# Performance work log

Measured on AMD Instinct MI355X. Metric: run time of the kernel, lower is better.

## Reference

```python
import jax, jax.numpy as jnp
import numpy as np

D_MODEL = 1024
NHEAD = 16
HEAD_DIM = D_MODEL // NHEAD
SCALE = 1.0 / np.sqrt(HEAD_DIM).astype(np.float32)
B, L = 2, 2048
NEG_INF = -1e30


def setup_inputs() -> dict:
    key = jax.random.key(0)
    ks = jax.random.split(key, 12)
    xav = np.sqrt(6.0 / (D_MODEL + D_MODEL)).astype(np.float32)  # xavier_uniform gain=1
    def lin_w(k):
        return jax.random.uniform(k, (D_MODEL, D_MODEL), jnp.float32, -xav, xav)
    x = jax.random.normal(ks[0], (B, L, D_MODEL), jnp.float32)
    role_mask = jax.random.randint(ks[1], (B, L), 0, 2, jnp.int32)
    # causal attention mask: True = masked (upper triangle above diagonal)
    attn_mask = jnp.triu(jnp.ones((L, L), jnp.bool_), k=1)
    # random key padding: True = padded key
    key_padding_mask = jax.random.randint(ks[2], (B, L), 0, 2, jnp.int32).astype(jnp.bool_)
    return {
        "x": x,
        "role_mask": role_mask,
        "attn_mask": attn_mask,
        "key_padding_mask": key_padding_mask,
        "Wq": lin_w(ks[3]), "bq": jnp.zeros((D_MODEL,), jnp.float32),
        "Wk": lin_w(ks[4]), "bk": jnp.zeros((D_MODEL,), jnp.float32),
        "Wv": lin_w(ks[5]), "bv": jnp.zeros((D_MODEL,), jnp.float32),
        "Wo": lin_w(ks[6]), "bo": jnp.zeros((D_MODEL,), jnp.float32),
        "delta": jnp.asarray(1.0, jnp.float32),
    }


def reference(x, role_mask, attn_mask, key_padding_mask,
              Wq, bq, Wk, bk, Wv, bv, Wo, bo, delta):
    Bb, Ll, Dd = x.shape
    def heads(t):  # [B,L,D] -> [B,H,L,hd]
        return t.reshape(Bb, Ll, NHEAD, HEAD_DIM).transpose(0, 2, 1, 3)
    Q = heads(x @ Wq.T + bq)
    K = heads(x @ Wk.T + bk)
    V = heads(x @ Wv.T + bv)
    scores = jnp.einsum('bhqd,bhkd->bhqk', Q, K) * SCALE  # [B,H,L,L]
    same_role = (role_mask[:, :, None] == role_mask[:, None, :])  # [B,L,L]
    scores = scores + (same_role.astype(scores.dtype) * delta)[:, None, :, :]
    scores = jnp.where(attn_mask[None, None, :, :], -jnp.inf, scores)
    scores = jnp.where(key_padding_mask[:, None, None, :], -jnp.inf, scores)
    attn = jax.nn.softmax(scores, axis=-1)
    attn = jnp.nan_to_num(attn, nan=0.0, posinf=0.0, neginf=0.0)
    out = jnp.einsum('bhqk,bhkd->bhqd', attn, V)
    out = out.transpose(0, 2, 1, 3).reshape(Bb, Ll, Dd)
    return out @ Wo.T + bo
```

## Files before the change

kernel.cpp:

```cpp
#include <hip/hip_runtime.h>
#include <hip/hip_bf16.h>

#define DM 1024
#define NH 16
#define HD 64
#define BB 2
#define LL 2048
#define SCALE 0.125f
#define NEG_BIG -1e30f
#define LOG2E 1.4426950408889634f
#define SC2 (SCALE * LOG2E)
#define FIXM 16.0f
#define SLOTB 8448
#define POOL0_SLOTS 960

typedef __bf16 bf16;
typedef __bf16 bf16x8 __attribute__((ext_vector_type(8)));
typedef __bf16 bf16x4 __attribute__((ext_vector_type(4)));
typedef float f32x4 __attribute__((ext_vector_type(4)));

static __device__ inline bf16x8 load8(const bf16* p) {
    return *reinterpret_cast<const bf16x8*>(p);
}

static __device__ inline float scrub(float x) {
    union { float f; unsigned u; } c; c.f = x;
    return ((c.u & 0x7F800000u) == 0x7F800000u) ? 0.f : x;
}

typedef __attribute__((address_space(1))) const unsigned char ga_t;
typedef __attribute__((address_space(3))) unsigned char ls_t;
static __device__ inline void gload_lds16(const void* g, void* l) {
    __builtin_amdgcn_global_load_lds((ga_t*)g, (ls_t*)l, 16, 0, 0);
}

__global__ __launch_bounds__(256) void prep_all(
    const float* __restrict__ x,
    const float* __restrict__ Wq, const float* __restrict__ Wk,
    const float* __restrict__ Wv, const float* __restrict__ Wo,
    bf16* __restrict__ xb, bf16* __restrict__ Wqb, bf16* __restrict__ Wkb,
    bf16* __restrict__ Wvb, bf16* __restrict__ Wob,
    const int* __restrict__ role, const void* __restrict__ kpad,
    const float* __restrict__ deltap, float2* __restrict__ biasG)
{
    const int tid = threadIdx.x;
    const int gid = blockIdx.x;
    if (gid < 2048) {
        const float* src; bf16* dst; size_t base;
        if (gid < 1024) { src = x; dst = xb; base = (size_t)gid * 1024; }
        else {
            const int wsel = (gid - 1024) >> 8;
            src = (wsel == 0) ? Wq : (wsel == 1) ? Wk : (wsel == 2) ? Wv : Wo;
            dst = (wsel == 0) ? Wqb : (wsel == 1) ? Wkb : (wsel == 2) ? Wvb : Wob;
            base = (size_t)((gid - 1024) & 255) * 1024;
        }
#pragma unroll
        for (int it = 0; it < 4; it++) {
            const size_t i = base + it * 256 + tid;
            const f32x4 v = ((const f32x4*)src)[i];
            bf16x4 o;
            o[0] = (bf16)v[0]; o[1] = (bf16)v[1]; o[2] = (bf16)v[2]; o[3] = (bf16)v[3];
            ((bf16x4*)dst)[i] = o;
        }
        return;
    }
    const unsigned char* kb = (const unsigned char*)kpad;
    int f3F = 0, fLow = 0, fOff = 0;
    for (int i = (tid & 63); i < BB * LL; i += 64) {
        const unsigned char v = kb[i];
        if (v == 0x3F) f3F = 1;
        if ((i & 3) < 2 && v) fLow = 1;
        if ((i & 3) && v) fOff = 1;
    }
    const int mode = __any(f3F) ? (__any(fLow) ? 3 : 2) : (__any(fOff) ? 1 : 0);
    const float d2 = scrub(deltap[0]) * LOG2E;
    const int idx = (gid - 2048) * 256 + tid;
    const bool pad = (mode == 0) ? (((const int*)kpad)[idx] != 0)
                   : (mode == 1) ? (((const unsigned char*)kpad)[idx] != 0)
                   : (mode == 2) ? (((const float*)kpad)[idx] != 0.f)
                                 : (((const unsigned short*)kpad)[idx] != 0);
    const int r = role[idx];
    const float base = (pad ? NEG_BIG : 0.f) - FIXM;
    float2 o;
    o.x = base + ((r == 0) ? d2 : 0.f);
    o.y = base + ((r == 1) ? d2 : 0.f);
    biasG[idx] = o;
}

__global__ __launch_bounds__(256) void qkv_bf16(
    const bf16* __restrict__ xb,
    const bf16* __restrict__ Wqb, const bf16* __restrict__ Wkb, const bf16* __restrict__ Wvb,
    const float* __restrict__ bq, const float* __restrict__ bk, const float* __restrict__ bv,
    bf16* __restrict__ qw, bf16* __restrict__ kw, bf16* __restrict__ vw)
{
    __shared__ bf16 As[128 * 32];
    __shared__ bf16 Bs[128 * 32];
    const int tid = threadIdx.x;
    const int lane = tid & 63, w = tid >> 6;
    const int wm = w >> 1, wn = w & 1;
    const int ln = lane & 15, quad = lane >> 4;

    const int m0 = blockIdx.x * 128;
    const int sel = blockIdx.y >> 3;
    const int nloc0 = (blockIdx.y & 7) * 128;

    const bf16* Wb = (sel == 0) ? Wqb : ((sel == 1) ? Wkb : Wvb);
    const float* bias = (sel == 0) ? bq : ((sel == 1) ? bk : bv);
    bf16* dstw = (sel == 0) ? qw : ((sel == 1) ? kw : vw);

    const int rA = lane >> 2;
    const int cA = (lane & 3) * 8;

    f32x4 acc[4][4] = {};
    for (int k0 = 0; k0 < DM; k0 += 32) {
        __syncthreads();
#pragma unroll
        for (int s = 0; s < 2; s++) {
            const int r0 = s * 64 + w * 16;
            gload_lds16(xb + (size_t)(m0 + r0 + rA) * DM + k0 + cA, &As[r0 * 32]);
            gload_lds16(Wb + (size_t)(nloc0 + r0 + rA) * DM + k0 + cA, &Bs[r0 * 32]);
        }
        __syncthreads();
        bf16x8 a[4], b[4];
#pragma unroll
        for (int mi = 0; mi < 4; mi++)
            a[mi] = *(bf16x8*)&As[(wm * 64 + mi * 16 + ln) * 32 + quad * 8];
#pragma unroll
        for (int ni = 0; ni < 4; ni++)
            b[ni] = *(bf16x8*)&Bs[(wn * 64 + ni * 16 + ln) * 32 + quad * 8];
#pragma unroll
        for (int mi = 0; mi < 4; mi++)
#pragma unroll
            for (int ni = 0; ni < 4; ni++)
                acc[mi][ni] = __builtin_amdgcn_mfma_f32_16x16x32_bf16(a[mi], b[ni], acc[mi][ni], 0, 0, 0);
    }

#pragma unroll
    for (int mi = 0; mi < 4; mi++) {
#pragma unroll
        for (int ni = 0; ni < 4; ni++) {
            const int ncol = nloc0 + wn * 64 + ni * 16 + ln;
            const float bv_ = bias[ncol];
            const int hh = ncol >> 6, dd = ncol & 63;
#pragma unroll
            for (int i = 0; i < 4; i++) {
                const int row = m0 + wm * 64 + mi * 16 + quad * 4 + i;
                const int bb = row >> 11, llr = row & (LL - 1);
                const bf16 v = (bf16)scrub(acc[mi][ni][i] + bv_);
                dstw[(((size_t)(bb * NH + hh) * LL) + llr) * HD + dd] = v;
            }
        }
    }
}

__global__ __launch_bounds__(256) void vtrans(
    const bf16* __restrict__ vw, bf16* __restrict__ vtw)
{
    __shared__ bf16 T[64][72];
    const int l0 = blockIdx.x * 64;
    const int bh = blockIdx.y;
    const int tid = threadIdx.x;
#pragma unroll
    for (int it = 0; it < 2; it++) {
        const int idx = it * 256 + tid;
        const int row = idx >> 3, c8 = (idx & 7) * 8;
        *(bf16x8*)&T[row][c8] = load8(vw + ((size_t)bh * LL + l0 + row) * HD + c8);
    }
    __syncthreads();
#pragma unroll
    for (int it = 0; it < 2; it++) {
        const int idx = it * 256 + tid;
        const int dd = idx >> 3, pg = (idx & 7) * 8;
        bf16x8 o;
#pragma unroll
        for (int j = 0; j < 8; j++) {
            const int p = pg + j;
            const int kl = (p & 3) * 16 + (p >> 2);
            o[j] = T[kl][dd];
        }
        *(bf16x8*)(vtw + ((size_t)bh * HD + dd) * LL + l0 + pg) = o;
    }
}

#define PSTR 32
__global__ __launch_bounds__(256) void attn_v11(
    const bf16* __restrict__ qw, const bf16* __restrict__ kw, const bf16* __restrict__ vtw,
    const int* __restrict__ role, const float2* __restrict__ biasG,
    char* __restrict__ pool0, char* __restrict__ pool1,
    bf16* __restrict__ attn_out)
{
    const int xg = blockIdx.x;
    int qb, c;
    if (xg < 24)      { qb = 31 - xg / 3; c = xg % 3; }
    else if (xg < 48) { qb = 23 - (xg - 24) / 2; c = (xg - 24) % 2; }
    else              { qb = 59 - xg; c = 0; }
    const int nch = (qb + 12) / 12;

    __shared__ bf16 Ks[2][2][64 * 32];
    __shared__ bf16 Vs[2][2][64 * 32];
    __shared__ bf16 Ps[4][2][16 * PSTR];

    const int tid = threadIdx.x;
    const int lane = tid & 63, w = tid >> 6;
    const int col = lane & 15, quad = lane >> 4;
    const int bh = blockIdx.y;
    const int h = bh & (NH - 1), b = bh >> 4;
    const int q0 = qb * 64 + w * 16;

    const bf16* qbase = qw + (size_t)((b * NH + h) * LL) * HD;
    const bf16* kbase = kw + (size_t)((b * NH + h) * LL) * HD;
    const bf16* vbase = vtw + (size_t)((b * NH + h) * HD) * LL;
    const float2* bias2 = biasG + (size_t)b * LL;
    const int* rrow = role + b * LL;

    const int srow = lane >> 2;
    const int scol = (lane & 3) * 8;
    const bf16* ksrc = kbase + (size_t)(w * 16 + srow) * HD + scol;
    const bf16* vsrc = vbase + (size_t)(w * 16 + srow) * LL + scol;

    bf16x8 qf[2];
    qf[0] = load8(qbase + (size_t)(q0 + col) * HD + quad * 8);
    qf[1] = load8(qbase + (size_t)(q0 + col) * HD + 32 + quad * 8);

    bf16x8 ones;
#pragma unroll
    for (int j = 0; j < 8; j++) ones[j] = (bf16)1.0f;

    int role_q[4];
#pragma unroll
    for (int i = 0; i < 4; i++) role_q[i] = rrow[q0 + quad * 4 + i];

    f32x4 ol = {};
    f32x4 o[4] = {};

    const int t0 = c * 12;
    const int t1 = (t0 + 12 < qb + 1) ? t0 + 12 : qb + 1;

    {
        const int kp = t0 * 64;
#pragma unroll
        for (int st = 0; st < 2; st++)
            gload_lds16(ksrc + (size_t)kp * HD + st * 32, &Ks[0][st][w * 512]);
#pragma unroll
        for (int kh = 0; kh < 2; kh++)
            gload_lds16(vsrc + kp + kh * 32, &Vs[0][kh][w * 512]);
    }

    const int wsw = (quad & 1) * 32;
    const int rsw = (col & 4) * 8;

    for (int kt = t0; kt < t1; kt++) {
        const int cur = (kt - t0) & 1;
        __syncthreads();

        if (kt + 1 < t1) {
            const int k1 = (kt + 1) * 64;
#pragma unroll
            for (int st = 0; st < 2; st++)
                gload_lds16(ksrc + (size_t)k1 * HD + st * 32, &Ks[cur ^ 1][st][w * 512]);
#pragma unroll
            for (int kh = 0; kh < 2; kh++)
                gload_lds16(vsrc + k1 + kh * 32, &Vs[cur ^ 1][kh][w * 512]);
        }

        const int k0 = kt * 64;
        float2 bb[4];
#pragma unroll
        for (int ns = 0; ns < 4; ns++) bb[ns] = bias2[k0 + ns * 16 + col];

        f32x4 s[4] = {};
#pragma unroll
        for (int st = 0; st < 2; st++) {
#pragma unroll
            for (int ns = 0; ns < 4; ns++) {
                const bf16x8 kf = *(bf16x8*)&Ks[cur][st][(ns * 16 + col) * 32 + quad * 8];
                s[ns] = __builtin_amdgcn_mfma_f32_16x16x32_bf16(qf[st], kf, s[ns], 0, 0, 0);
            }
        }
        const bool diag = (kt == qb);
        const int half = col >> 3;
        const int poff = (col & 7) * 4;
#pragma unroll
        for (int i = 0; i < 4; i++) {
            bf16x4 pk;
#pragma unroll
            for (int ns = 0; ns < 4; ns++) {
                float sv = fmaf(s[ns][i], SC2, role_q[i] ? bb[ns].y : bb[ns].x);
                if (diag && (k0 + ns * 16 + col) > q0 + quad * 4 + i) sv = NEG_BIG;
                pk[ns] = (bf16)exp2f(sv);
            }
            *(bf16x4*)&Ps[w][half][(((quad * 4 + i) * PSTR + poff) ^ wsw)] = pk;
        }
        bf16x8 pf[2];
#pragma unroll
        for (int st = 0; st < 2; st++)
            pf[st] = *(bf16x8*)&Ps[w][st][(col * PSTR + quad * 8) ^ rsw];
#pragma unroll
        for (int ns = 0; ns < 4; ns++) {
#pragma unroll
            for (int kh = 0; kh < 2; kh++) {
                const bf16x8 vf = *(bf16x8*)&Vs[cur][kh][(ns * 16 + col) * 32 + quad * 8];
                o[ns] = __builtin_amdgcn_mfma_f32_16x16x32_bf16(pf[kh], vf, o[ns], 0, 0, 0);
            }
        }
#pragma unroll
        for (int kh = 0; kh < 2; kh++)
            ol = __builtin_amdgcn_mfma_f32_16x16x32_bf16(pf[kh], ones, ol, 0, 0, 0);
    }

    if (nch == 1) {
        bf16* orow = attn_out + (size_t)(b * LL) * DM;
#pragma unroll
        for (int i = 0; i < 4; i++) {
            const float l = ol[i];
            const float inv = (l > 0.f) ? 1.f / l : 0.f;
            const int qq = q0 + quad * 4 + i;
#pragma unroll
            for (int ns = 0; ns < 4; ns++)
                orow[(size_t)qq * DM + h * HD + ns * 16 + col] = (bf16)scrub(o[ns][i] * inv);
        }
    } else {
        const int base = (qb <= 23) ? (qb - 12) * 2 : 24 + (qb - 24) * 3;
        const int slot = bh * 48 + base + c;
        char* ptr = (slot < POOL0_SLOTS) ? (pool0 + (size_t)slot * SLOTB)
                                         : (pool1 + (size_t)(slot - POOL0_SLOTS) * SLOTB);
        bf16* op = (bf16*)ptr;
        float* lp = (float*)(ptr + 8192);
#pragma unroll
        for (int i = 0; i < 4; i++) {
            const int r = w * 16 + quad * 4 + i;
            if (col == 0) lp[r] = ol[i];
#pragma unroll
            for (int ns = 0; ns < 4; ns++)
                op[r * 64 + ns * 16 + col] = (bf16)scrub(o[ns][i]);
        }
    }
}

__global__ __launch_bounds__(256) void combine(
    const char* __restrict__ pool0, const char* __restrict__ pool1,
    bf16* __restrict__ attn_out)
{
    const int qb = 12 + blockIdx.x;
    const int bh = blockIdx.y;
    const int h = bh & (NH - 1), b = bh >> 4;
    const int nch = (qb + 12) / 12;
    const int base = (qb <= 23) ? (qb - 12) * 2 : 24 + (qb - 24) * 3;

    const char* ptr[3];
    for (int c = 0; c < nch; c++) {
        const int slot = bh * 48 + base + c;
        ptr[c] = (slot < POOL0_SLOTS) ? (pool0 + (size_t)slot * SLOTB)
                                      : (pool1 + (size_t)(slot - POOL0_SLOTS) * SLOTB);
    }

    __shared__ float linv[64];
    const int tid = threadIdx.x;
    if (tid < 64) {
        float ls = 0.f;
        for (int c = 0; c < nch; c++) ls += ((const float*)(ptr[c] + 8192))[tid];
        linv[tid] = (ls > 0.f) ? 1.f / ls : 0.f;
    }
    __syncthreads();

    const int r = tid >> 2;
    const int d0 = (tid & 3) * 16;
    float acc[16] = {};
    for (int c = 0; c < nch; c++) {
        const bf16* op = (const bf16*)ptr[c];
#pragma unroll
        for (int half = 0; half < 2; half++) {
            const bf16x8 v = load8(op + r * 64 + d0 + half * 8);
#pragma unroll
            for (int j = 0; j < 8; j++) acc[half * 8 + j] += (float)v[j];
        }
    }
    const float inv = linv[r];
    bf16x8 outv[2];
#pragma unroll
    for (int half = 0; half < 2; half++)
#pragma unroll
        for (int j = 0; j < 8; j++)
            outv[half][j] = (bf16)scrub(acc[half * 8 + j] * inv);
    bf16* orow = attn_out + ((size_t)(b * LL) + qb * 64 + r) * DM + h * HD + d0;
    *(bf16x8*)orow = outv[0];
    *(bf16x8*)(orow + 8) = outv[1];
}

__global__ __launch_bounds__(256) void out_bf16(
    const bf16* __restrict__ A, const bf16* __restrict__ Wb,
    const float* __restrict__ bias, float* __restrict__ out)
{
    __shared__ bf16 As[128 * 32];
    __shared__ bf16 Bs[64 * 32];
    const int tid = threadIdx.x;
    const int lane = tid & 63, w = tid >> 6;
    const int ln = lane & 15, quad = lane >> 4;
    const int m0 = blockIdx.x * 128;
    const int n0 = blockIdx.y * 64;

    const int rA = lane >> 2;
    const int cA = (lane & 3) * 8;

    f32x4 acc[2][4] = {};
    for (int k0 = 0; k0 < DM; k0 += 32) {
        __syncthreads();
#pragma unroll
        for (int s = 0; s < 2; s++) {
            const int r0 = s * 64 + w * 16;
            gload_lds16(A + (size_t)(m0 + r0 + rA) * DM + k0 + cA, &As[r0 * 32]);
        }
        gload_lds16(Wb + (size_t)(n0 + w * 16 + rA) * DM + k0 + cA, &Bs[w * 16 * 32]);
        __syncthreads();
        bf16x8 a[2], b[4];
#pragma unroll
        for (int mi = 0; mi < 2; mi++)
            a[mi] = *(bf16x8*)&As[(w * 32 + mi * 16 + ln) * 32 + quad * 8];
#pragma unroll
        for (int ni = 0; ni < 4; ni++)
            b[ni] = *(bf16x8*)&Bs[(ni * 16 + ln) * 32 + quad * 8];
#pragma unroll
        for (int mi = 0; mi < 2; mi++)
#pragma unroll
            for (int ni = 0; ni < 4; ni++)
                acc[mi][ni] = __builtin_amdgcn_mfma_f32_16x16x32_bf16(a[mi], b[ni], acc[mi][ni], 0, 0, 0);
    }
#pragma unroll
    for (int mi = 0; mi < 2; mi++) {
#pragma unroll
        for (int ni = 0; ni < 4; ni++) {
            const int ncol = n0 + ni * 16 + ln;
            const float bv_ = bias[ncol];
#pragma unroll
            for (int i = 0; i < 4; i++) {
                const int row = m0 + w * 32 + mi * 16 + quad * 4 + i;
                out[(size_t)row * DM + ncol] = scrub(acc[mi][ni][i] + bv_);
            }
        }
    }
}

extern "C" void kernel_launch(void* const* d_in, const int* in_sizes, int n_in,
                              void* d_out, int out_size, void* d_ws, size_t ws_size,
                              hipStream_t stream) {
    const float* x    = (const float*)d_in[0];
    const int*   role = (const int*)d_in[1];
    const void*  kpad = d_in[3];
    const float* Wq = (const float*)d_in[4];
    const float* bq = (const float*)d_in[5];
    const float* Wk = (const float*)d_in[6];
    const float* bk = (const float*)d_in[7];
    const float* Wv = (const float*)d_in[8];
    const float* bv = (const float*)d_in[9];
    const float* Wo = (const float*)d_in[10];
    const float* bo = (const float*)d_in[11];
    const float* dl = (const float*)d_in[12];

    char* ws = (char*)d_ws;
    bf16* qw   = (bf16*)(ws);
    bf16* kw   = (bf16*)(ws + (size_t)(8u  << 20));
    bf16* Wqb  = (bf16*)(ws + (size_t)(16u << 20));
    bf16* Wkb  = (bf16*)(ws + (size_t)(18u << 20));
    bf16* Wvb  = (bf16*)(ws + (size_t)(20u << 20));
    char* pool0 = ws + (size_t)(16u << 20);
    bf16* vw   = (bf16*)(ws + (size_t)(24u << 20));
    bf16* aw   = (bf16*)(ws + (size_t)(24u << 20));
    bf16* vtw  = (bf16*)(ws + (size_t)(32u << 20));
    bf16* xb   = (bf16*)(ws + (size_t)(40u << 20));
    char* pool1 = ws + (size_t)(40u << 20);
    bf16* Wob  = (bf16*)(ws + (size_t)(48u << 20) + 65536);
    float2* biasG = (float2*)(ws + (size_t)(48u << 20));
    float* out = (float*)d_out;

    prep_all<<<dim3(2064), dim3(256), 0, stream>>>(
        x, Wq, Wk, Wv, Wo, xb, Wqb, Wkb, Wvb, Wob, role, kpad, dl, biasG);
    qkv_bf16<<<dim3(32, 24), dim3(256), 0, stream>>>(
        xb, Wqb, Wkb, Wvb, bq, bk, bv, qw, kw, vw);
    vtrans<<<dim3(32, 32), dim3(256), 0, stream>>>(vw, vtw);
    attn_v11<<<dim3(60, 32), dim3(256), 0, stream>>>(
        qw, kw, vtw, role, biasG, pool0, pool1, aw);
    combine<<<dim3(20, 32), dim3(256), 0, stream>>>(pool0, pool1, aw);
    out_bf16<<<dim3(32, 16), dim3(256), 0, stream>>>(aw, Wob, bo, out);
}
```

Baseline: 233.6 us.

## Remap blocks across XCDs for L2 locality and swizzle attention LDS tiles

Block indices in the QKV GEMM, output GEMM and attention kernels are remapped so that blocks sharing the same input rows, or the same batch-head, land on the same XCD (lin & 7). The goal is better L2 reuse on MI355X's chiplet layout. The attention kernel also switches to an XOR swizzle of the K/V global-to-LDS load columns and the P staging buffer, aiming to cut LDS bank conflicts on the MFMA operand reads. The remapping depends on the hardware dispatching blocks round-robin across XCDs, and the swizzle indices must stay consistent between writers and readers.

```diff
diff --git a/kernel.cpp b/kernel.cpp
--- a/kernel.cpp
+++ b/kernel.cpp
@@ -100,9 +100,14 @@
     const int wm = w >> 1, wn = w & 1;
     const int ln = lane & 15, quad = lane >> 4;
 
-    const int m0 = blockIdx.x * 128;
-    const int sel = blockIdx.y >> 3;
-    const int nloc0 = (blockIdx.y & 7) * 128;
+    const int lin = blockIdx.y * 32 + blockIdx.x;
+    const int xcd = lin & 7;
+    const int t = lin >> 3;
+    const int mloc = t & 3;
+    const int yy = t >> 2;
+    const int m0 = (xcd * 4 + mloc) * 128;
+    const int sel = yy >> 3;
+    const int nloc0 = (yy & 7) * 128;
 
     const bf16* Wb = (sel == 0) ? Wqb : ((sel == 1) ? Wkb : Wvb);
     const float* bias = (sel == 0) ? bq : ((sel == 1) ? bk : bv);
@@ -183,13 +188,19 @@
 }
 
 #define PSTR 32
-__global__ __launch_bounds__(256) void attn_v11(
+__global__ __launch_bounds__(256) void attn_v12(
     const bf16* __restrict__ qw, const bf16* __restrict__ kw, const bf16* __restrict__ vtw,
     const int* __restrict__ role, const float2* __restrict__ biasG,
     char* __restrict__ pool0, char* __restrict__ pool1,
     bf16* __restrict__ attn_out)
 {
-    const int xg = blockIdx.x;
+    const int lin = blockIdx.y * 60 + blockIdx.x;
+    const int xcd = lin & 7;
+    const int t = lin >> 3;
+    const int xg = t % 60;
+    const int g = t / 60;
+    const int bh = g * 8 + xcd;
+
     int qb, c;
     if (xg < 24)      { qb = 31 - xg / 3; c = xg % 3; }
     else if (xg < 48) { qb = 23 - (xg - 24) / 2; c = (xg - 24) % 2; }
@@ -203,7 +214,6 @@
     const int tid = threadIdx.x;
     const int lane = tid & 63, w = tid >> 6;
     const int col = lane & 15, quad = lane >> 4;
-    const int bh = blockIdx.y;
     const int h = bh & (NH - 1), b = bh >> 4;
     const int q0 = qb * 64 + w * 16;
 
@@ -214,9 +224,9 @@
     const int* rrow = role + b * LL;
 
     const int srow = lane >> 2;
-    const int scol = (lane & 3) * 8;
-    const bf16* ksrc = kbase + (size_t)(w * 16 + srow) * HD + scol;
-    const bf16* vsrc = vbase + (size_t)(w * 16 + srow) * LL + scol;
+    const int swz = ((lane & 3) ^ ((lane >> 3) & 3)) * 8;
+    const bf16* ksrc = kbase + (size_t)(w * 16 + srow) * HD + swz;
+    const bf16* vsrc = vbase + (size_t)(w * 16 + srow) * LL + swz;
 
     bf16x8 qf[2];
     qf[0] = load8(qbase + (size_t)(q0 + col) * HD + quad * 8);
@@ -246,8 +256,7 @@
             gload_lds16(vsrc + kp + kh * 32, &Vs[0][kh][w * 512]);
     }
 
-    const int wsw = (quad & 1) * 32;
-    const int rsw = (col & 4) * 8;
+    const int rs = (quad ^ ((col >> 1) & 3)) * 8;
 
     for (int kt = t0; kt < t1; kt++) {
         const int cur = (kt - t0) & 1;
@@ -273,13 +282,12 @@
         for (int st = 0; st < 2; st++) {
 #pragma unroll
             for (int ns = 0; ns < 4; ns++) {
-                const bf16x8 kf = *(bf16x8*)&Ks[cur][st][(ns * 16 + col) * 32 + quad * 8];
+                const bf16x8 kf = *(bf16x8*)&Ks[cur][st][(ns * 16 + col) * 32 + rs];
                 s[ns] = __builtin_amdgcn_mfma_f32_16x16x32_bf16(qf[st], kf, s[ns], 0, 0, 0);
             }
         }
         const bool diag = (kt == qb);
         const int half = col >> 3;
-        const int poff = (col & 7) * 4;
 #pragma unroll
         for (int i = 0; i < 4; i++) {
             bf16x4 pk;
@@ -289,17 +297,20 @@
                 if (diag && (k0 + ns * 16 + col) > q0 + quad * 4 + i) sv = NEG_BIG;
                 pk[ns] = (bf16)exp2f(sv);
             }
-            *(bf16x4*)&Ps[w][half][(((quad * 4 + i) * PSTR + poff) ^ wsw)] = pk;
+            const int row = quad * 4 + i;
+            const int sw = (quad * 2 + (i >> 1)) & 3;
+            const int ew = ((((col & 7) >> 1) ^ sw) * 8) + (col & 1) * 4;
+            *(bf16x4*)&Ps[w][half][row * PSTR + ew] = pk;
         }
         bf16x8 pf[2];
 #pragma unroll
         for (int st = 0; st < 2; st++)
-            pf[st] = *(bf16x8*)&Ps[w][st][(col * PSTR + quad * 8) ^ rsw];
+            pf[st] = *(bf16x8*)&Ps[w][st][col * PSTR + rs];
 #pragma unroll
         for (int ns = 0; ns < 4; ns++) {
 #pragma unroll
             for (int kh = 0; kh < 2; kh++) {
-                const bf16x8 vf = *(bf16x8*)&Vs[cur][kh][(ns * 16 + col) * 32 + quad * 8];
+                const bf16x8 vf = *(bf16x8*)&Vs[cur][kh][(ns * 16 + col) * 32 + rs];
                 o[ns] = __builtin_amdgcn_mfma_f32_16x16x32_bf16(pf[kh], vf, o[ns], 0, 0, 0);
             }
         }
@@ -396,8 +407,14 @@
     const int tid = threadIdx.x;
     const int lane = tid & 63, w = tid >> 6;
     const int ln = lane & 15, quad = lane >> 4;
-    const int m0 = blockIdx.x * 128;
-    const int n0 = blockIdx.y * 64;
+
+    const int lin = blockIdx.y * 32 + blockIdx.x;
+    const int xcd = lin & 7;
+    const int t = lin >> 3;
+    const int mloc = t & 3;
+    const int n = t >> 2;
+    const int m0 = (xcd * 4 + mloc) * 128;
+    const int n0 = n * 64;
 
     const int rA = lane >> 2;
     const int cA = (lane & 3) * 8;
@@ -477,7 +494,7 @@
     qkv_bf16<<<dim3(32, 24), dim3(256), 0, stream>>>(
         xb, Wqb, Wkb, Wvb, bq, bk, bv, qw, kw, vw);
     vtrans<<<dim3(32, 32), dim3(256), 0, stream>>>(vw, vtw);
-    attn_v11<<<dim3(60, 32), dim3(256), 0, stream>>>(
+    attn_v12<<<dim3(60, 32), dim3(256), 0, stream>>>(
         qw, kw, vtw, role, biasG, pool0, pool1, aw);
     combine<<<dim3(20, 32), dim3(256), 0, stream>>>(pool0, pool1, aw);
     out_bf16<<<dim3(32, 16), dim3(256), 0, stream>>>(aw, Wob, bo, out);
```

New measurement: 225.6 us. -3.4%, faster.
